# Kernel optimization log

Measured on AMD Instinct MI355X. Metric: run time of the kernel, lower is better.

Reference implementation:

```python
import jax, jax.numpy as jnp
import numpy as np

ALPHA = 0.7
NUM_HEADS = 12
NUM_KV_HEADS = 6
HEAD_DIM = 64
ROPE_BASE = 10000.0


def ternary_quantize(w):
    thr = ALPHA * jnp.mean(jnp.abs(w))
    return jnp.sign(w) * (jnp.abs(w) >= thr).astype(w.dtype)


def bitlinear(x, w):
    # forward: F.linear(x, ternary(w)) * mean(|w|)
    scale = jnp.mean(jnp.abs(w))
    qw = ternary_quantize(w)
    return (x @ qw.T) * scale


def rope_tables(seq_len, dim, dtype):
    inv_freq = 1.0 / (ROPE_BASE ** (jnp.arange(0, dim, 2, dtype=jnp.float32) / dim))
    t = jnp.arange(seq_len, dtype=jnp.float32)
    freqs = jnp.outer(t, inv_freq)            # [S, dim/2]
    emb = jnp.concatenate([freqs, freqs], -1)  # [S, dim]
    return jnp.cos(emb).astype(dtype), jnp.sin(emb).astype(dtype)


def rotate_half(x):
    x1, x2 = jnp.split(x, 2, axis=-1)
    return jnp.concatenate([-x2, x1], axis=-1)


def setup_inputs() -> dict:
    key = jax.random.key(0)
    ks = jax.random.split(key, 5)
    B, S, H = 2, 2048, 768
    return {
        "hidden_states": jax.random.normal(ks[0], (B, S, H), jnp.float32),
        "Wq": jax.random.normal(ks[1], (768, 768), jnp.float32) * 0.02,
        "Wk": jax.random.normal(ks[2], (384, 768), jnp.float32) * 0.02,
        "Wv": jax.random.normal(ks[3], (384, 768), jnp.float32) * 0.02,
        "Wo": jax.random.normal(ks[4], (768, 768), jnp.float32) * 0.02,
    }


def reference(hidden_states, Wq, Wk, Wv, Wo):
    B, S, H = hidden_states.shape
    nh, nkv, hd = NUM_HEADS, NUM_KV_HEADS, HEAD_DIM
    groups = nh // nkv

    q = bitlinear(hidden_states, Wq).reshape(B, S, nh, hd).transpose(0, 2, 1, 3)
    k = bitlinear(hidden_states, Wk).reshape(B, S, nkv, hd).transpose(0, 2, 1, 3)
    v = bitlinear(hidden_states, Wv).reshape(B, S, nkv, hd).transpose(0, 2, 1, 3)

    cos, sin = rope_tables(S, hd, hidden_states.dtype)  # [S, hd]
    cos = cos[None, None]  # [1,1,S,hd]
    sin = sin[None, None]
    q = q * cos + rotate_half(q) * sin
    k = k * cos + rotate_half(k) * sin

    # GQA: expand kv heads to full head count
    k = jnp.repeat(k, groups, axis=1)  # [B, nh, S, hd]
    v = jnp.repeat(v, groups, axis=1)

    scale = 1.0 / jnp.sqrt(jnp.asarray(hd, hidden_states.dtype))
    scores = jnp.einsum("bhsd,bhtd->bhst", q, k) * scale
    attn = jax.nn.softmax(scores, axis=-1)
    out = jnp.einsum("bhst,bhtd->bhsd", attn, v)
    out = out.transpose(0, 2, 1, 3).reshape(B, S, H)
    return bitlinear(out, Wo)
```

## Files before the change

### kernel.cpp

```cpp
#include <hip/hip_runtime.h>
#include <cmath>

typedef unsigned short u16;
typedef unsigned int u32;
typedef __bf16 bf16x2 __attribute__((ext_vector_type(2)));
typedef __bf16 bf16x8 __attribute__((ext_vector_type(8)));
typedef float f32x16 __attribute__((ext_vector_type(16)));

#define NQ (768*768)
#define NK (384*768)

__device__ __forceinline__ u16 f2bf(float f) {
  u32 u = __float_as_uint(f);
  u32 r = (u + 0x7FFFu + ((u >> 16) & 1u)) >> 16;
  return (u16)r;
}
__device__ __forceinline__ u32 packbf(float a, float b) {
#if __has_builtin(__builtin_amdgcn_cvt_pk_bf16_f32)
  bf16x2 v = __builtin_amdgcn_cvt_pk_bf16_f32(a, b);
  u32 r; __builtin_memcpy(&r, &v, 4); return r;
#else
  return (u32)f2bf(a) | ((u32)f2bf(b) << 16);
#endif
}
__device__ __forceinline__ float fexp2(float x) {
#if __has_builtin(__builtin_amdgcn_exp2f)
  return __builtin_amdgcn_exp2f(x);
#else
  return exp2f(x);
#endif
}
__device__ __forceinline__ bf16x8 ldfrag(const u16* p) { bf16x8 v; __builtin_memcpy(&v, p, 16); return v; }
__device__ __forceinline__ f32x16 mfma32_(bf16x8 a, bf16x8 b, f32x16 c) {
  return __builtin_amdgcn_mfma_f32_32x32x16_bf16(a, b, c, 0, 0, 0);
}

__device__ __forceinline__ int fidx(int r, int k) {
  return (r >> 5) * 24576 + (k >> 4) * 512 + ((r & 31) + 32 * ((k >> 3) & 1)) * 8 + (k & 7);
}
__device__ __forceinline__ int kidx(int b6kvh, int s, int d) {
  return b6kvh * 131072 + (s >> 5) * 2048 + (d >> 4) * 512 +
         ((s & 31) + 32 * ((d >> 3) & 1)) * 8 + (d & 7);
}
__device__ __forceinline__ int qidx(int b, int s, int h, int d) {
  return ((b * 64 + (s >> 5)) * 12 + h) * 2048 + (d >> 4) * 512 +
         ((s & 31) + 32 * ((d >> 3) & 1)) * 8 + (d & 7);
}
__device__ __forceinline__ int vidx(int b6kvh, int d, int p) {
  return b6kvh * 131072 + (p >> 6) * 4096 + (d >> 5) * 2048 + ((p >> 4) & 3) * 512 +
         ((d & 31) + 32 * ((p >> 3) & 1)) * 8 + (p & 7);
}

__global__ __launch_bounds__(256) void abssum_kernel(const float* __restrict__ wq, const float* __restrict__ wk,
                                                     const float* __restrict__ wv, const float* __restrict__ wo,
                                                     float* __restrict__ sums) {
  int which = blockIdx.y;
  const float* w = (which == 0) ? wq : (which == 1) ? wk : (which == 2) ? wv : wo;
  int n4 = ((which == 0 || which == 3) ? NQ : NK) >> 2;
  const float4* w4 = (const float4*)w;
  float s = 0.f;
  for (int i = blockIdx.x * blockDim.x + threadIdx.x; i < n4; i += gridDim.x * blockDim.x) {
    float4 v = w4[i];
    s += fabsf(v.x) + fabsf(v.y) + fabsf(v.z) + fabsf(v.w);
  }
  for (int off = 32; off; off >>= 1) s += __shfl_down(s, off);
  __shared__ float ls[4];
  if ((threadIdx.x & 63) == 0) ls[threadIdx.x >> 6] = s;
  __syncthreads();
  if (threadIdx.x == 0) atomicAdd(&sums[which], ls[0] + ls[1] + ls[2] + ls[3]);
}

__global__ __launch_bounds__(256) void prep_kernel(const float* __restrict__ wq, const float* __restrict__ wk,
                                                   const float* __restrict__ wv, const float* __restrict__ wo,
                                                   const float* __restrict__ sums, const float* __restrict__ x,
                                                   u16* __restrict__ qw, u16* __restrict__ woq,
                                                   u16* __restrict__ xb, float2* __restrict__ rt) {
  int i = blockIdx.x * blockDim.x + threadIdx.x;
  if (i < 221184) {
    int n = i / 96, k8 = i - n * 96;
    const float* src; float th; u16* dst; int nd;
    if (n < 768)       { src = wq + n * 768;          th = 0.7f * sums[0] * (1.f / NQ); dst = qw;  nd = n; }
    else if (n < 1152) { src = wk + (n - 768) * 768;  th = 0.7f * sums[1] * (1.f / NK); dst = qw;  nd = n; }
    else if (n < 1536) { src = wv + (n - 1152) * 768; th = 0.7f * sums[2] * (1.f / NK); dst = qw;  nd = n; }
    else               { src = wo + (n - 1536) * 768; th = 0.7f * sums[3] * (1.f / NQ); dst = woq; nd = n - 1536; }
    const float4* sp = (const float4*)(src + k8 * 8);
    float4 v0 = sp[0], v1 = sp[1];
    float e[8] = {v0.x, v0.y, v0.z, v0.w, v1.x, v1.y, v1.z, v1.w};
    u16 o[8];
#pragma unroll
    for (int j = 0; j < 8; j++)
      o[j] = f2bf((fabsf(e[j]) >= th) ? ((e[j] > 0.f) ? 1.f : -1.f) : 0.f);
    __builtin_memcpy(dst + fidx(nd, k8 * 8), o, 16);
  } else if (i < 614400) {
    int j = i - 221184;
    int m = j / 96, k8 = j - m * 96;
    const float4* xp = (const float4*)(x + m * 768 + k8 * 8);
    float4 v0 = xp[0], v1 = xp[1];
    u16 o[8] = { f2bf(v0.x), f2bf(v0.y), f2bf(v0.z), f2bf(v0.w),
                 f2bf(v1.x), f2bf(v1.y), f2bf(v1.z), f2bf(v1.w) };
    __builtin_memcpy(xb + fidx(m, k8 * 8), o, 16);
  } else {
    int j = i - 614400;
    int s = j >> 5, c = j & 31;
    float f = exp2f((float)c * -0.41524101186092029f);
    float sn, cs; sincosf((float)s * f, &sn, &cs);
    rt[j] = make_float2(cs, sn);
  }
}

__global__ __launch_bounds__(256, 3) void gemm_qkv_kernel(const u16* __restrict__ xb, const u16* __restrict__ qw,
                                                          const float* __restrict__ sums,
                                                          const float2* __restrict__ rt,
                                                          u16* __restrict__ qb, u16* __restrict__ kb,
                                                          u16* __restrict__ vT) {
  int tn = blockIdx.x, tm = blockIdx.y;
  int t = threadIdx.x, lane = t & 63, w = t >> 6, c = lane & 31, g2 = lane >> 5;
  int wm = w & 1, wn = w >> 1;
  const u16* abase = xb + (tm * 2 + wm) * 24576 + lane * 8;
  const u16* bbase0 = qw + (tn * 4 + wn * 2) * 24576 + lane * 8;
  const u16* bbase1 = bbase0 + 24576;
  f32x16 acc[2]; acc[0] = (f32x16)0.f; acc[1] = (f32x16)0.f;
  bf16x8 aA[4], c0A[4], c1A[4], aB[4], c0B[4], c1B[4];
#pragma unroll
  for (int ks = 0; ks < 4; ks++) {
    aA[ks]  = ldfrag(abase + ks * 512);
    c0A[ks] = ldfrag(bbase0 + ks * 512);
    c1A[ks] = ldfrag(bbase1 + ks * 512);
  }
#pragma unroll
  for (int kk = 0; kk < 48; kk += 8) {
#pragma unroll
    for (int ks = 0; ks < 4; ks++) {
      aB[ks]  = ldfrag(abase + (kk + 4 + ks) * 512);
      c0B[ks] = ldfrag(bbase0 + (kk + 4 + ks) * 512);
      c1B[ks] = ldfrag(bbase1 + (kk + 4 + ks) * 512);
    }
#pragma unroll
    for (int ks = 0; ks < 4; ks++) {
      acc[0] = mfma32_(aA[ks], c0A[ks], acc[0]);
      acc[1] = mfma32_(aA[ks], c1A[ks], acc[1]);
    }
    if (kk + 8 < 48) {
#pragma unroll
      for (int ks = 0; ks < 4; ks++) {
        aA[ks]  = ldfrag(abase + (kk + 8 + ks) * 512);
        c0A[ks] = ldfrag(bbase0 + (kk + 8 + ks) * 512);
        c1A[ks] = ldfrag(bbase1 + (kk + 8 + ks) * 512);
      }
    }
#pragma unroll
    for (int ks = 0; ks < 4; ks++) {
      acc[0] = mfma32_(aB[ks], c0B[ks], acc[0]);
      acc[1] = mfma32_(aB[ks], c1B[ks], acc[1]);
    }
  }
  float sq = sums[0] * (1.f / NQ) * 0.180336880111120f;
  float sk = sums[1] * (1.f / NK);
  float sv = sums[2] * (1.f / NK);
  int mb = tm * 64 + wm * 32 + 4 * g2;
  if (tn < 9) {
    float sc = (tn < 6) ? sq : sk;
    int head = (tn < 6) ? (tn * 2 + wn) : ((tn - 6) * 2 + wn);
    const float2* rp = rt + c;
#pragma unroll
    for (int r = 0; r < 16; r++) {
      int m = mb + (r & 3) + 8 * (r >> 2);
      int bb = m >> 11, s = m & 2047;
      float2 cs2 = rp[s << 5];
      float x1 = acc[0][r] * sc, x2 = acc[1][r] * sc;
      u16 y1 = f2bf(x1 * cs2.x - x2 * cs2.y);
      u16 y2 = f2bf(x2 * cs2.x + x1 * cs2.y);
      if (tn < 6) {
        qb[qidx(bb, s, head, c)]      = y1;
        qb[qidx(bb, s, head, c + 32)] = y2;
      } else {
        kb[kidx(bb * 6 + head, s, c)]      = y1;
        kb[kidx(bb * 6 + head, s, c + 32)] = y2;
      }
    }
  } else {
    int kvh = (tn - 9) * 2 + wn;
#pragma unroll
    for (int nb = 0; nb < 2; nb++)
#pragma unroll
      for (int r = 0; r < 16; r++) {
        int m = mb + (r & 3) + 8 * (r >> 2);
        int bb = m >> 11, s = m & 2047;
        int sp = (s & ~12) | ((s & 4) << 1) | ((s & 8) >> 1);
        vT[vidx(bb * 6 + kvh, nb * 32 + c, sp)] = f2bf(acc[nb][r] * sv);
      }
  }
}

__device__ __forceinline__ void load_k4(bf16x8 (&kf)[4], const u16* Kb, int grp, int lane) {
  const u16* kt = Kb + grp * 2048 + lane * 8;
#pragma unroll
  for (int ks = 0; ks < 4; ks++) kf[ks] = ldfrag(kt + ks * 512);
}
__device__ __forceinline__ void load_v4(bf16x8 (&vf)[2][2], const u16* Vb, int grp, int lane) {
  const u16* vt = Vb + (grp >> 1) * 4096 + (grp & 1) * 1024 + lane * 8;
  vf[0][0] = ldfrag(vt);
  vf[0][1] = ldfrag(vt + 512);
  vf[1][0] = ldfrag(vt + 2048);
  vf[1][1] = ldfrag(vt + 2048 + 512);
}
__device__ __forceinline__ void attn_step(const bf16x8 (&kf)[4], const bf16x8 (&vf)[2][2],
                                          const bf16x8 (&qf)[4], f32x16 (&O)[2], float& lsum) {
  f32x16 S = (f32x16)0.f;
#pragma unroll
  for (int ks = 0; ks < 4; ks++) S = mfma32_(kf[ks], qf[ks], S);
#pragma unroll
  for (int r = 0; r < 16; r++) S[r] = fexp2(S[r]);
  lsum += (((S[0] + S[1]) + (S[2] + S[3])) + ((S[4] + S[5]) + (S[6] + S[7])))
        + (((S[8] + S[9]) + (S[10] + S[11])) + ((S[12] + S[13]) + (S[14] + S[15])));
  u32 P[8];
#pragma unroll
  for (int j = 0; j < 8; j++) P[j] = packbf(S[2 * j], S[2 * j + 1]);
  bf16x8 PA0, PA1;
  __builtin_memcpy(&PA0, &P[0], 16);
  __builtin_memcpy(&PA1, &P[4], 16);
  O[0] = mfma32_(PA0, vf[0][0], O[0]);
  O[1] = mfma32_(PA0, vf[1][0], O[1]);
  O[0] = mfma32_(PA1, vf[0][1], O[0]);
  O[1] = mfma32_(PA1, vf[1][1], O[1]);
}

__global__ __launch_bounds__(256, 3) void attn_kernel(const u16* __restrict__ qb, const u16* __restrict__ kb,
                                                      const u16* __restrict__ vT, u16* __restrict__ ab) {
  __shared__ float Obuf[4][32][66];
  __shared__ float Lbuf[4][32];
  int bk = blockIdx.x, qt = blockIdx.y;
  int b = bk / 6, kvh = bk % 6;
  int t = threadIdx.x, lane = t & 63, w = t >> 6, c = lane & 31, g2 = lane >> 5;
  int qn = w & 1, kh = w >> 1;

  const u16* qbase = qb + ((b * 64 + qt) * 12 + kvh * 2 + qn) * 2048;
  bf16x8 qf[4];
#pragma unroll
  for (int ks = 0; ks < 4; ks++) qf[ks] = ldfrag(qbase + ks * 512 + lane * 8);

  f32x16 fz = (f32x16)0.f;
  f32x16 O[2] = {fz, fz};
  float lsum = 0.f;

  const u16* Kb = kb + bk * 131072;
  const u16* Vb = vT + bk * 131072;

  bf16x8 kfA[4], kfB[4], vfA[2][2], vfB[2][2];
  int g = kh * 32;
  load_k4(kfA, Kb, g, lane);
  load_v4(vfA, Vb, g, lane);
  for (int it2 = 0; it2 < 16; ++it2) {
    load_k4(kfB, Kb, g + 1, lane);
    load_v4(vfB, Vb, g + 1, lane);
    attn_step(kfA, vfA, qf, O, lsum);
    if (it2 < 15) {
      load_k4(kfA, Kb, g + 2, lane);
      load_v4(vfA, Vb, g + 2, lane);
    }
    attn_step(kfB, vfB, qf, O, lsum);
    g += 2;
  }
  float ltot = lsum + __shfl_xor(lsum, 32);
  if (g2 == 0) Lbuf[w][c] = ltot;
#pragma unroll
  for (int dn = 0; dn < 2; dn++)
#pragma unroll
    for (int r = 0; r < 16; r++)
      Obuf[w][(r & 3) + 8 * (r >> 2) + 4 * g2][dn * 32 + c] = O[dn][r];
  __syncthreads();
  {
    int hn = t >> 7, qq = (t >> 2) & 31, dc = (t & 3) * 16;
    float l = Lbuf[hn][qq] + Lbuf[hn + 2][qq];
    float inv = 1.f / l;
    u16 o[16];
#pragma unroll
    for (int j = 0; j < 16; j++)
      o[j] = f2bf((Obuf[hn][qq][dc + j] + Obuf[hn + 2][qq][dc + j]) * inv);
    int h = kvh * 2 + hn;
    int mg = b * 64 + qt;
    u16* dst = ab + mg * 24576 + ((h * 64 + dc) >> 4) * 512 + qq * 8;
    __builtin_memcpy(dst, o, 16);
    __builtin_memcpy(dst + 256, o + 8, 16);
  }
}

__global__ __launch_bounds__(256, 3) void gemm_out_kernel(const u16* __restrict__ ab, const u16* __restrict__ woq,
                                                          const float* __restrict__ sums, float* __restrict__ out) {
  int tn = blockIdx.x, tm = blockIdx.y;
  int t = threadIdx.x, lane = t & 63, w = t >> 6, c = lane & 31, g2 = lane >> 5;
  int wm = w & 1, wn = w >> 1;
  const u16* abase = ab + (tm * 2 + wm) * 24576 + lane * 8;
  const u16* bbase = woq + (tn * 2 + wn) * 24576 + lane * 8;
  f32x16 acc = (f32x16)0.f;
  bf16x8 aA[4], bA[4], aB[4], bB[4];
#pragma unroll
  for (int ks = 0; ks < 4; ks++) {
    aA[ks] = ldfrag(abase + ks * 512);
    bA[ks] = ldfrag(bbase + ks * 512);
  }
#pragma unroll
  for (int kk = 0; kk < 48; kk += 8) {
#pragma unroll
    for (int ks = 0; ks < 4; ks++) {
      aB[ks] = ldfrag(abase + (kk + 4 + ks) * 512);
      bB[ks] = ldfrag(bbase + (kk + 4 + ks) * 512);
    }
#pragma unroll
    for (int ks = 0; ks < 4; ks++) acc = mfma32_(aA[ks], bA[ks], acc);
    if (kk + 8 < 48) {
#pragma unroll
      for (int ks = 0; ks < 4; ks++) {
        aA[ks] = ldfrag(abase + (kk + 8 + ks) * 512);
        bA[ks] = ldfrag(bbase + (kk + 8 + ks) * 512);
      }
    }
#pragma unroll
    for (int ks = 0; ks < 4; ks++) acc = mfma32_(aB[ks], bB[ks], acc);
  }
  float so = sums[3] * (1.f / NQ);
  int mb = tm * 64 + wm * 32 + 4 * g2;
#pragma unroll
  for (int r = 0; r < 16; r++) {
    int m = mb + (r & 3) + 8 * (r >> 2);
    out[m * 768 + tn * 64 + wn * 32 + c] = acc[r] * so;
  }
}

extern "C" void kernel_launch(void* const* d_in, const int* in_sizes, int n_in,
                              void* d_out, int out_size, void* d_ws, size_t ws_size,
                              hipStream_t stream) {
  const float* x  = (const float*)d_in[0];
  const float* wq = (const float*)d_in[1];
  const float* wk = (const float*)d_in[2];
  const float* wv = (const float*)d_in[3];
  const float* wo = (const float*)d_in[4];
  float* out = (float*)d_out;
  char* ws = (char*)d_ws;

  float* sums = (float*)ws;
  u16* qw  = (u16*)(ws + 256);
  u16* woq = (u16*)(ws + 2359552);
  u16* xb  = (u16*)(ws + 3539200);
  u16* qb  = (u16*)(ws + 9830656);
  u16* kb  = (u16*)(ws + 16122112);
  u16* vT  = (u16*)(ws + 19267840);
  u16* ab  = (u16*)(ws + 22413568);
  float2* rt = (float2*)(ws + 28705024);

  hipMemsetAsync(sums, 0, 16, stream);
  dim3 blk(256);
  abssum_kernel<<<dim3(64, 4), blk, 0, stream>>>(wq, wk, wv, wo, sums);
  prep_kernel<<<dim3(2656), blk, 0, stream>>>(wq, wk, wv, wo, sums, x, qw, woq, xb, rt);
  gemm_qkv_kernel<<<dim3(12, 64), blk, 0, stream>>>(xb, qw, sums, rt, qb, kb, vT);
  attn_kernel<<<dim3(12, 64), blk, 0, stream>>>(qb, kb, vT, ab);
  gemm_out_kernel<<<dim3(12, 64), blk, 0, stream>>>(ab, woq, sums, out);
}
```

Before: 156.2 us.

## Stage K/V tiles through LDS with async global_load_lds double buffering

The attention kernel now loads K and V tiles cooperatively into a double-buffered LDS region using direct global-to-LDS loads. Each wave stages one quarter of the tile and all waves read fragments from LDS, so each K/V tile is shared across two query tiles. Block mapping changes to one query head per block covering two query tiles. The intent is to halve global K/V traffic per query and hide load latency. The cost is a __syncthreads per iteration and added LDS usage.

```diff
diff --git a/kernel.cpp b/kernel.cpp
--- a/kernel.cpp
+++ b/kernel.cpp
@@ -33,6 +33,10 @@
 __device__ __forceinline__ bf16x8 ldfrag(const u16* p) { bf16x8 v; __builtin_memcpy(&v, p, 16); return v; }
 __device__ __forceinline__ f32x16 mfma32_(bf16x8 a, bf16x8 b, f32x16 c) {
   return __builtin_amdgcn_mfma_f32_32x32x16_bf16(a, b, c, 0, 0, 0);
+}
+__device__ __forceinline__ void gload_lds16(const u16* g, u16* l) {
+  __builtin_amdgcn_global_load_lds((const __attribute__((address_space(1))) void*)g,
+                                   (__attribute__((address_space(3))) void*)l, 16, 0, 0);
 }
 
 __device__ __forceinline__ int fidx(int r, int k) {
@@ -192,76 +196,83 @@
   }
 }
 
-__device__ __forceinline__ void load_k4(bf16x8 (&kf)[4], const u16* Kb, int grp, int lane) {
-  const u16* kt = Kb + grp * 2048 + lane * 8;
-#pragma unroll
-  for (int ks = 0; ks < 4; ks++) kf[ks] = ldfrag(kt + ks * 512);
-}
-__device__ __forceinline__ void load_v4(bf16x8 (&vf)[2][2], const u16* Vb, int grp, int lane) {
-  const u16* vt = Vb + (grp >> 1) * 4096 + (grp & 1) * 1024 + lane * 8;
-  vf[0][0] = ldfrag(vt);
-  vf[0][1] = ldfrag(vt + 512);
-  vf[1][0] = ldfrag(vt + 2048);
-  vf[1][1] = ldfrag(vt + 2048 + 512);
-}
-__device__ __forceinline__ void attn_step(const bf16x8 (&kf)[4], const bf16x8 (&vf)[2][2],
-                                          const bf16x8 (&qf)[4], f32x16 (&O)[2], float& lsum) {
-  f32x16 S = (f32x16)0.f;
-#pragma unroll
-  for (int ks = 0; ks < 4; ks++) S = mfma32_(kf[ks], qf[ks], S);
-#pragma unroll
-  for (int r = 0; r < 16; r++) S[r] = fexp2(S[r]);
-  lsum += (((S[0] + S[1]) + (S[2] + S[3])) + ((S[4] + S[5]) + (S[6] + S[7])))
-        + (((S[8] + S[9]) + (S[10] + S[11])) + ((S[12] + S[13]) + (S[14] + S[15])));
-  u32 P[8];
-#pragma unroll
-  for (int j = 0; j < 8; j++) P[j] = packbf(S[2 * j], S[2 * j + 1]);
-  bf16x8 PA0, PA1;
-  __builtin_memcpy(&PA0, &P[0], 16);
-  __builtin_memcpy(&PA1, &P[4], 16);
-  O[0] = mfma32_(PA0, vf[0][0], O[0]);
-  O[1] = mfma32_(PA0, vf[1][0], O[1]);
-  O[0] = mfma32_(PA1, vf[0][1], O[0]);
-  O[1] = mfma32_(PA1, vf[1][1], O[1]);
-}
-
 __global__ __launch_bounds__(256, 3) void attn_kernel(const u16* __restrict__ qb, const u16* __restrict__ kb,
                                                       const u16* __restrict__ vT, u16* __restrict__ ab) {
-  __shared__ float Obuf[4][32][66];
-  __shared__ float Lbuf[4][32];
-  int bk = blockIdx.x, qt = blockIdx.y;
+  __shared__ __align__(16) char smb[34304];
+  u16* sm16 = (u16*)smb;
+  int bk = blockIdx.x;
   int b = bk / 6, kvh = bk % 6;
+  int qp = blockIdx.y & 31, h2 = blockIdx.y >> 5;
+  int h = kvh * 2 + h2;
   int t = threadIdx.x, lane = t & 63, w = t >> 6, c = lane & 31, g2 = lane >> 5;
-  int qn = w & 1, kh = w >> 1;
-
-  const u16* qbase = qb + ((b * 64 + qt) * 12 + kvh * 2 + qn) * 2048;
+  int qi = w & 1, kh = w >> 1;
+  int qt = qp * 2 + qi;
+
+  const u16* qbase = qb + ((b * 64 + qt) * 12 + h) * 2048;
   bf16x8 qf[4];
 #pragma unroll
   for (int ks = 0; ks < 4; ks++) qf[ks] = ldfrag(qbase + ks * 512 + lane * 8);
+
+  const u16* Kb = kb + bk * 131072;
+  const u16* Vb = vT + bk * 131072;
+
+  auto stage = [&](int it, int nb) {
+    u16* regb = sm16 + nb * 8192 + w * 2048;
+    int g = (w >> 1) * 32 + it;
+    if ((w & 1) == 0) {
+      const u16* sb = Kb + g * 2048 + lane * 8;
+#pragma unroll
+      for (int q = 0; q < 4; q++) gload_lds16(sb + q * 512, regb + q * 512);
+    } else {
+      const u16* sb = Vb + (g >> 1) * 4096 + (g & 1) * 1024 + lane * 8;
+#pragma unroll
+      for (int q = 0; q < 4; q++)
+        gload_lds16(sb + (q >> 1) * 2048 + (q & 1) * 512, regb + q * 512);
+    }
+  };
 
   f32x16 fz = (f32x16)0.f;
   f32x16 O[2] = {fz, fz};
   float lsum = 0.f;
 
-  const u16* Kb = kb + bk * 131072;
-  const u16* Vb = vT + bk * 131072;
-
-  bf16x8 kfA[4], kfB[4], vfA[2][2], vfB[2][2];
-  int g = kh * 32;
-  load_k4(kfA, Kb, g, lane);
-  load_v4(vfA, Vb, g, lane);
-  for (int it2 = 0; it2 < 16; ++it2) {
-    load_k4(kfB, Kb, g + 1, lane);
-    load_v4(vfB, Vb, g + 1, lane);
-    attn_step(kfA, vfA, qf, O, lsum);
-    if (it2 < 15) {
-      load_k4(kfA, Kb, g + 2, lane);
-      load_v4(vfA, Vb, g + 2, lane);
-    }
-    attn_step(kfB, vfB, qf, O, lsum);
-    g += 2;
-  }
+  stage(0, 0);
+  __syncthreads();
+  for (int it = 0; it < 32; ++it) {
+    int nb = it & 1;
+    if (it < 31) stage(it + 1, nb ^ 1);
+    const u16* kreg = sm16 + nb * 8192 + (kh * 2) * 2048;
+    const u16* vreg = kreg + 2048;
+    bf16x8 kf[4], vf[2][2];
+#pragma unroll
+    for (int ks = 0; ks < 4; ks++) kf[ks] = ldfrag(kreg + ks * 512 + lane * 8);
+#pragma unroll
+    for (int dn = 0; dn < 2; dn++)
+#pragma unroll
+      for (int ksv = 0; ksv < 2; ksv++)
+        vf[dn][ksv] = ldfrag(vreg + dn * 1024 + ksv * 512 + lane * 8);
+    f32x16 S = fz;
+#pragma unroll
+    for (int ks = 0; ks < 4; ks++) S = mfma32_(kf[ks], qf[ks], S);
+#pragma unroll
+    for (int r = 0; r < 16; r++) S[r] = fexp2(S[r]);
+    lsum += (((S[0] + S[1]) + (S[2] + S[3])) + ((S[4] + S[5]) + (S[6] + S[7])))
+          + (((S[8] + S[9]) + (S[10] + S[11])) + ((S[12] + S[13]) + (S[14] + S[15])));
+    u32 P[8];
+#pragma unroll
+    for (int j = 0; j < 8; j++) P[j] = packbf(S[2 * j], S[2 * j + 1]);
+    bf16x8 PA0, PA1;
+    __builtin_memcpy(&PA0, &P[0], 16);
+    __builtin_memcpy(&PA1, &P[4], 16);
+    O[0] = mfma32_(PA0, vf[0][0], O[0]);
+    O[1] = mfma32_(PA0, vf[1][0], O[1]);
+    O[0] = mfma32_(PA1, vf[0][1], O[0]);
+    O[1] = mfma32_(PA1, vf[1][1], O[1]);
+    __syncthreads();
+  }
+
   float ltot = lsum + __shfl_xor(lsum, 32);
+  float (*Obuf)[32][66] = (float(*)[32][66])smb;
+  float (*Lbuf)[32] = (float(*)[32])(smb + 33792);
   if (g2 == 0) Lbuf[w][c] = ltot;
 #pragma unroll
   for (int dn = 0; dn < 2; dn++)
@@ -277,8 +288,7 @@
 #pragma unroll
     for (int j = 0; j < 16; j++)
       o[j] = f2bf((Obuf[hn][qq][dc + j] + Obuf[hn + 2][qq][dc + j]) * inv);
-    int h = kvh * 2 + hn;
-    int mg = b * 64 + qt;
+    int mg = b * 64 + qp * 2 + hn;
     u16* dst = ab + mg * 24576 + ((h * 64 + dc) >> 4) * 512 + qq * 8;
     __builtin_memcpy(dst, o, 16);
     __builtin_memcpy(dst + 256, o + 8, 16);
```

New measurement: 158.6 us. About the same (+1.5%).
